# Performance work log

Measured on AMD Instinct MI355X. Metric: run time of the kernel, lower is better.

## Reference

```python
import jax, jax.numpy as jnp
import numpy as np

B, C, H, W = 32, 256, 56, 56
G, K, RED = 2, 7, 4
BN_EPS = 1e-5


def _conv2d(x, w, pad, groups=1, bias=None):
    # x: (N, Cin, H, W), w: (Cout, Cin/groups, kh, kw)
    y = jax.lax.conv_general_dilated(
        x, w, window_strides=(1, 1), padding=[(pad, pad), (pad, pad)],
        dimension_numbers=("NCHW", "OIHW", "NCHW"), feature_group_count=groups)
    if bias is not None:
        y = y + bias[None, :, None, None]
    return y


def setup_inputs() -> dict:
    key = jax.random.key(0)
    ks = jax.random.split(key, 5)
    return {
        "x": jax.random.normal(ks[0], (B, C, H, W), jnp.float32),
        "w_dyn": jax.random.normal(ks[1], (G, C, K, K), jnp.float32) * 0.02,
        "proj1_w": jax.random.normal(ks[2], (C // RED, C, 3, 3), jnp.float32) * 0.02,
        "bn_gamma": jnp.ones((C // RED,), jnp.float32),
        "bn_beta": jnp.zeros((C // RED,), jnp.float32),
        "proj2_w": jax.random.normal(ks[3], (C * G, C // RED, 3, 3), jnp.float32) * 0.02,
        "proj2_b": jnp.zeros((C * G,), jnp.float32),
    }


def reference(x, w_dyn, proj1_w, bn_gamma, bn_beta, proj2_w, proj2_b):
    b, c, h, w = x.shape
    # AdaptiveAvgPool2d((K, K)); H, W divisible by K -> exact mean over (H//K, W//K) windows
    pooled = x.reshape(b, c, K, h // K, K, w // K).mean(axis=(3, 5))  # (B, C, K, K)
    # proj: Conv3x3 (no bias, BN follows) -> BN (inference: mean=0, var=1) -> GELU -> Conv3x3
    hmid = _conv2d(pooled, proj1_w, pad=1)
    hmid = hmid * (bn_gamma / jnp.sqrt(1.0 + BN_EPS))[None, :, None, None] + bn_beta[None, :, None, None]
    hmid = jax.nn.gelu(hmid, approximate=False)
    scale = _conv2d(hmid, proj2_w, pad=1, bias=proj2_b)  # (B, G*C, K, K)
    scale = jax.nn.softmax(scale.reshape(b, G, c, K, K), axis=1)
    # per-sample dynamic depthwise kernel: softmax-weighted mix of G kernel banks
    dyn_w = jnp.einsum("bgckl,gckl->bckl", scale, w_dyn)  # (B, C, K, K)
    # depthwise conv with per-sample weights: groups = B*C
    y = _conv2d(x.reshape(1, b * c, h, w), dyn_w.reshape(b * c, 1, K, K),
                pad=K // 2, groups=b * c)
    return y.reshape(b, c, h, w)
```

## Files before the change

kernel.cpp:

```cpp
#include <hip/hip_runtime.h>
#include <math.h>

#define BB 32
#define CC 256
#define HH 56
#define WW 56
#define KP 49
#define CMID 64
#define HW 3136

#define RSTR 64
#define PROWS 62
#define PSZ (PROWS * RSTR)

__global__ __launch_bounds__(256) void pre_kernel(const float* __restrict__ x,
                                                  const float* __restrict__ w1,
                                                  const float* __restrict__ w2,
                                                  float* __restrict__ pooled,
                                                  float* __restrict__ w1t,
                                                  float* __restrict__ w2t) {
    int bid = blockIdx.x;
    if (bid < 2048) {
        int wv = threadIdx.x >> 6, lane = threadIdx.x & 63;
        int g = bid * 4 + wv;
        if (lane < KP) {
            int ko = lane / 7, kw = lane - ko * 7;
            const float* base = x + (size_t)g * HW + (ko * 8) * WW + kw * 8;
            float s = 0.f;
            #pragma unroll
            for (int r = 0; r < 8; ++r) {
                float4 a = *(const float4*)(base + r * WW);
                float4 b4 = *(const float4*)(base + r * WW + 4);
                s += a.x + a.y + a.z + a.w + b4.x + b4.y + b4.z + b4.w;
            }
            pooled[(size_t)g * KP + lane] = s * (1.f / 64.f);
        }
        return;
    }
    __shared__ float t[64][65];
    int r = threadIdx.x >> 6, c = threadIdx.x & 63;
    if (bid < 2048 + 36) {
        int ct0 = (bid - 2048) * 64;
        #pragma unroll
        for (int i = 0; i < 16; ++i)
            t[r + 4 * i][c] = w1[(size_t)(r + 4 * i) * 2304 + ct0 + c];
        __syncthreads();
        #pragma unroll
        for (int i = 0; i < 16; ++i)
            w1t[(size_t)(ct0 + r + 4 * i) * 64 + c] = t[c][r + 4 * i];
    } else {
        int tt = bid - 2048 - 36;
        int co0 = (tt / 9) * 64, ct0 = (tt % 9) * 64;
        #pragma unroll
        for (int i = 0; i < 16; ++i)
            t[r + 4 * i][c] = w2[(size_t)(co0 + r + 4 * i) * 576 + ct0 + c];
        __syncthreads();
        #pragma unroll
        for (int i = 0; i < 16; ++i)
            w2t[(size_t)(ct0 + r + 4 * i) * 512 + co0 + c] = t[c][r + 4 * i];
    }
}

__global__ __launch_bounds__(512) void conv1_kernel(const float* __restrict__ pooled,
                                                    const float* __restrict__ w1t,
                                                    const float* __restrict__ gamma,
                                                    const float* __restrict__ beta,
                                                    float* __restrict__ hmid) {
    int y = blockIdx.x, b = blockIdx.y;
    int wv = threadIdx.x >> 6, co = threadIdx.x & 63;
    __shared__ float red[8][7][64];
    float acc[7] = {0.f, 0.f, 0.f, 0.f, 0.f, 0.f, 0.f};
    const float* pb = pooled + (size_t)b * CC * KP;
    for (int ci = 0; ci < 32; ++ci) {
        int cin = wv * 32 + ci;
        const float* prow_base = pb + cin * KP;
        const float* wbase = w1t + (size_t)(cin * 9) * 64 + co;
        #pragma unroll
        for (int ky = 0; ky < 3; ++ky) {
            int iy = y + ky - 1;
            if (0 <= iy && iy < 7) {
                float s[9];
                s[0] = 0.f; s[8] = 0.f;
                const float* pr = prow_base + iy * 7;
                #pragma unroll
                for (int j = 0; j < 7; ++j) s[j + 1] = pr[j];
                const float* wr = wbase + ky * 3 * 64;
                float w0 = wr[0], w1v = wr[64], w2v = wr[128];
                #pragma unroll
                for (int xx = 0; xx < 7; ++xx)
                    acc[xx] += s[xx] * w0 + s[xx + 1] * w1v + s[xx + 2] * w2v;
            }
        }
    }
    #pragma unroll
    for (int xx = 0; xx < 7; ++xx) red[wv][xx][co] = acc[xx];
    __syncthreads();
    if (threadIdx.x < 448) {
        int xx = threadIdx.x >> 6, c2 = threadIdx.x & 63;
        float tot = 0.f;
        #pragma unroll
        for (int w = 0; w < 8; ++w) tot += red[w][xx][c2];
        float bnscale = gamma[c2] * rsqrtf(1.f + 1e-5f);
        float h = tot * bnscale + beta[c2];
        float g = 0.5f * h * (1.f + erff(h * 0.70710678118654752440f));
        hmid[((size_t)b * CMID + c2) * KP + y * 7 + xx] = g;
    }
}

__global__ __launch_bounds__(512) void conv2_kernel(const float* __restrict__ hmid,
                                                    const float* __restrict__ w2t,
                                                    const float* __restrict__ b2,
                                                    const float* __restrict__ wdyn,
                                                    float* __restrict__ dynw) {
    int y = blockIdx.x, b = blockIdx.y;
    int g = threadIdx.x >> 8, co = threadIdx.x & 255;
    __shared__ float redA[2][7][256];
    __shared__ float redB[2][7][256];
    float a0[7] = {}, a1[7] = {};
    const float* hb = hmid + (size_t)b * CMID * KP;
    for (int ci = 0; ci < 32; ++ci) {
        int cin = g * 32 + ci;
        const float* hrow_base = hb + cin * KP;
        const float* wbase = w2t + (size_t)(cin * 9) * 512 + co;
        #pragma unroll
        for (int ky = 0; ky < 3; ++ky) {
            int iy = y + ky - 1;
            if (0 <= iy && iy < 7) {
                float s[9];
                s[0] = 0.f; s[8] = 0.f;
                const float* hr = hrow_base + iy * 7;
                #pragma unroll
                for (int j = 0; j < 7; ++j) s[j + 1] = hr[j];
                const float* wr = wbase + ky * 3 * 512;
                float wa0 = wr[0],    wb0 = wr[256];
                float wa1 = wr[512],  wb1 = wr[768];
                float wa2 = wr[1024], wb2 = wr[1280];
                #pragma unroll
                for (int xx = 0; xx < 7; ++xx) {
                    float v0 = s[xx], v1 = s[xx + 1], v2 = s[xx + 2];
                    a0[xx] += v0 * wa0 + v1 * wa1 + v2 * wa2;
                    a1[xx] += v0 * wb0 + v1 * wb1 + v2 * wb2;
                }
            }
        }
    }
    #pragma unroll
    for (int xx = 0; xx < 7; ++xx) { redA[g][xx][co] = a0[xx]; redB[g][xx][co] = a1[xx]; }
    __syncthreads();
    if (threadIdx.x < 256) {
        int c = threadIdx.x;
        float bias0 = b2[c], bias1 = b2[c + CC];
        const float* wd0 = wdyn + (size_t)c * KP + y * 7;
        const float* wd1 = wdyn + (size_t)(CC + c) * KP + y * 7;
        float* dw = dynw + ((size_t)(b * CC + c)) * KP + y * 7;
        #pragma unroll
        for (int xx = 0; xx < 7; ++xx) {
            float s0 = redA[0][xx][c] + redA[1][xx][c] + bias0;
            float s1 = redB[0][xx][c] + redB[1][xx][c] + bias1;
            float m = fmaxf(s0, s1);
            float e0 = expf(s0 - m), e1 = expf(s1 - m);
            dw[xx] = (e0 * wd0[xx] + e1 * wd1[xx]) / (e0 + e1);
        }
    }
}

__global__ __launch_bounds__(64, 4) void dwconv_kernel(const float* __restrict__ x,
                                                       const float* __restrict__ dynw,
                                                       float* __restrict__ out) {
    __shared__ __align__(16) float xs[PSZ];
    int tid = threadIdx.x;
    int g = blockIdx.x;

    const float* wp = dynw + (size_t)g * KP;
    float w[49];
    #pragma unroll
    for (int i = 0; i < 49; ++i) w[i] = wp[i];

    for (int idx = tid; idx < 208; idx += 64) {
        int pr, col;
        if (idx < 96) {
            int rowi = idx >> 4, c4 = idx & 15;
            pr = rowi < 3 ? rowi : rowi + 56;
            col = 4 * c4;
        } else {
            int i = idx - 96;
            int rr = i >> 1;
            pr = rr + 3;
            int shift = 4 * (pr & 7);
            col = (i & 1) ? ((shift + 60) & 63) : shift;
        }
        *(float4*)(xs + pr * RSTR + col) = make_float4(0.f, 0.f, 0.f, 0.f);
    }

    for (int idx = tid; idx < 784; idx += 64) {
        int rr = idx / 14, c4 = idx - rr * 14;
        float4 v = *((const float4*)(x + (size_t)g * HW + rr * WW) + c4);
        int pr = rr + 3;
        int shift = 4 * (pr & 7);
        int col = (4 * c4 + 4 + shift) & 63;
        *(float4*)(xs + pr * RSTR + col) = v;
    }
    __syncthreads();

    if (tid < 56) {
        int ty = tid / 7, tx = tid - ty * 7;
        int r0 = 7 * ty, c0 = 8 * tx;
        float acc[7][8] = {};
        #pragma unroll
        for (int ir = 0; ir < 13; ++ir) {
            int pr = r0 + ir;
            int shift = 4 * (pr & 7);
            const float* rowp = xs + pr * RSTR;
            float rb[16];
            #pragma unroll
            for (int k = 0; k < 4; ++k) {
                int col = (c0 + shift + 4 * k) & 63;
                float4 v = *(const float4*)(rowp + col);
                rb[4 * k + 0] = v.x; rb[4 * k + 1] = v.y;
                rb[4 * k + 2] = v.z; rb[4 * k + 3] = v.w;
            }
            #pragma unroll
            for (int ky = 0; ky < 7; ++ky) {
                int oy = ir - ky;
                if (0 <= oy && oy < 7) {
                    #pragma unroll
                    for (int kx = 0; kx < 7; ++kx) {
                        float ww = w[ky * 7 + kx];
                        #pragma unroll
                        for (int ox = 0; ox < 8; ++ox)
                            acc[oy][ox] += rb[ox + 1 + kx] * ww;
                    }
                }
            }
        }
        float* op = out + (size_t)g * HW;
        #pragma unroll
        for (int oy = 0; oy < 7; ++oy) {
            float* orow = op + (r0 + oy) * WW + c0;
            *(float4*)(orow)     = make_float4(acc[oy][0], acc[oy][1], acc[oy][2], acc[oy][3]);
            *(float4*)(orow + 4) = make_float4(acc[oy][4], acc[oy][5], acc[oy][6], acc[oy][7]);
        }
    }
}

extern "C" void kernel_launch(void* const* d_in, const int* in_sizes, int n_in,
                              void* d_out, int out_size, void* d_ws, size_t ws_size,
                              hipStream_t stream) {
    const float* x     = (const float*)d_in[0];
    const float* wdyn  = (const float*)d_in[1];
    const float* w1    = (const float*)d_in[2];
    const float* gamma = (const float*)d_in[3];
    const float* beta  = (const float*)d_in[4];
    const float* w2    = (const float*)d_in[5];
    const float* b2    = (const float*)d_in[6];
    float* out = (float*)d_out;

    float* ws     = (float*)d_ws;
    float* pooled = ws;
    float* hmid   = ws + 401408;
    float* dynw   = ws + 501760;
    float* w1t    = ws + 903168;
    float* w2t    = ws + 1050624;

    pre_kernel   <<<dim3(2048 + 36 + 72), 256, 0, stream>>>(x, w1, w2, pooled, w1t, w2t);
    conv1_kernel <<<dim3(7, BB),          512, 0, stream>>>(pooled, w1t, gamma, beta, hmid);
    conv2_kernel <<<dim3(7, BB),          512, 0, stream>>>(hmid, w2t, b2, wdyn, dynw);
    dwconv_kernel<<<dim3(BB * CC),         64, 0, stream>>>(x, dynw, out);
}
```

Baseline: 321.0 us.

## Read depthwise input directly from global memory; double conv block threads

```diff
diff --git a/kernel.cpp b/kernel.cpp
--- a/kernel.cpp
+++ b/kernel.cpp
@@ -8,10 +8,6 @@
 #define KP 49
 #define CMID 64
 #define HW 3136
-
-#define RSTR 64
-#define PROWS 62
-#define PSZ (PROWS * RSTR)
 
 __global__ __launch_bounds__(256) void pre_kernel(const float* __restrict__ x,
                                                   const float* __restrict__ w1,
@@ -61,18 +57,20 @@
     }
 }
 
-__global__ __launch_bounds__(512) void conv1_kernel(const float* __restrict__ pooled,
-                                                    const float* __restrict__ w1t,
-                                                    const float* __restrict__ gamma,
-                                                    const float* __restrict__ beta,
-                                                    float* __restrict__ hmid) {
+__global__ __launch_bounds__(1024) void conv1_kernel(const float* __restrict__ pooled,
+                                                     const float* __restrict__ w1t,
+                                                     const float* __restrict__ gamma,
+                                                     const float* __restrict__ beta,
+                                                     float* __restrict__ hmid) {
     int y = blockIdx.x, b = blockIdx.y;
     int wv = threadIdx.x >> 6, co = threadIdx.x & 63;
-    __shared__ float red[8][7][64];
+    __shared__ float red[16][7][64];
     float acc[7] = {0.f, 0.f, 0.f, 0.f, 0.f, 0.f, 0.f};
     const float* pb = pooled + (size_t)b * CC * KP;
-    for (int ci = 0; ci < 32; ++ci) {
-        int cin = wv * 32 + ci;
+    int cin0 = __builtin_amdgcn_readfirstlane(wv * 16);
+    #pragma unroll 4
+    for (int ci = 0; ci < 16; ++ci) {
+        int cin = cin0 + ci;
         const float* prow_base = pb + cin * KP;
         const float* wbase = w1t + (size_t)(cin * 9) * 64 + co;
         #pragma unroll
@@ -99,7 +97,7 @@
         int xx = threadIdx.x >> 6, c2 = threadIdx.x & 63;
         float tot = 0.f;
         #pragma unroll
-        for (int w = 0; w < 8; ++w) tot += red[w][xx][c2];
+        for (int w = 0; w < 16; ++w) tot += red[w][xx][c2];
         float bnscale = gamma[c2] * rsqrtf(1.f + 1e-5f);
         float h = tot * bnscale + beta[c2];
         float g = 0.5f * h * (1.f + erff(h * 0.70710678118654752440f));
@@ -107,19 +105,21 @@
     }
 }
 
-__global__ __launch_bounds__(512) void conv2_kernel(const float* __restrict__ hmid,
-                                                    const float* __restrict__ w2t,
-                                                    const float* __restrict__ b2,
-                                                    const float* __restrict__ wdyn,
-                                                    float* __restrict__ dynw) {
+__global__ __launch_bounds__(1024) void conv2_kernel(const float* __restrict__ hmid,
+                                                     const float* __restrict__ w2t,
+                                                     const float* __restrict__ b2,
+                                                     const float* __restrict__ wdyn,
+                                                     float* __restrict__ dynw) {
     int y = blockIdx.x, b = blockIdx.y;
-    int g = threadIdx.x >> 8, co = threadIdx.x & 255;
-    __shared__ float redA[2][7][256];
-    __shared__ float redB[2][7][256];
+    int qq = threadIdx.x >> 8, co = threadIdx.x & 255;
+    __shared__ float redA[4][7][256];
+    __shared__ float redB[4][7][256];
     float a0[7] = {}, a1[7] = {};
     const float* hb = hmid + (size_t)b * CMID * KP;
-    for (int ci = 0; ci < 32; ++ci) {
-        int cin = g * 32 + ci;
+    int cin0 = __builtin_amdgcn_readfirstlane(qq * 16);
+    #pragma unroll 2
+    for (int ci = 0; ci < 16; ++ci) {
+        int cin = cin0 + ci;
         const float* hrow_base = hb + cin * KP;
         const float* wbase = w2t + (size_t)(cin * 9) * 512 + co;
         #pragma unroll
@@ -145,7 +145,7 @@
         }
     }
     #pragma unroll
-    for (int xx = 0; xx < 7; ++xx) { redA[g][xx][co] = a0[xx]; redB[g][xx][co] = a1[xx]; }
+    for (int xx = 0; xx < 7; ++xx) { redA[qq][xx][co] = a0[xx]; redB[qq][xx][co] = a1[xx]; }
     __syncthreads();
     if (threadIdx.x < 256) {
         int c = threadIdx.x;
@@ -155,8 +155,8 @@
         float* dw = dynw + ((size_t)(b * CC + c)) * KP + y * 7;
         #pragma unroll
         for (int xx = 0; xx < 7; ++xx) {
-            float s0 = redA[0][xx][c] + redA[1][xx][c] + bias0;
-            float s1 = redB[0][xx][c] + redB[1][xx][c] + bias1;
+            float s0 = redA[0][xx][c] + redA[1][xx][c] + redA[2][xx][c] + redA[3][xx][c] + bias0;
+            float s1 = redB[0][xx][c] + redB[1][xx][c] + redB[2][xx][c] + redB[3][xx][c] + bias1;
             float m = fmaxf(s0, s1);
             float e0 = expf(s0 - m), e1 = expf(s1 - m);
             dw[xx] = (e0 * wd0[xx] + e1 * wd1[xx]) / (e0 + e1);
@@ -167,7 +167,6 @@
 __global__ __launch_bounds__(64, 4) void dwconv_kernel(const float* __restrict__ x,
                                                        const float* __restrict__ dynw,
                                                        float* __restrict__ out) {
-    __shared__ __align__(16) float xs[PSZ];
     int tid = threadIdx.x;
     int g = blockIdx.x;
 
@@ -176,46 +175,24 @@
     #pragma unroll
     for (int i = 0; i < 49; ++i) w[i] = wp[i];
 
-    for (int idx = tid; idx < 208; idx += 64) {
-        int pr, col;
-        if (idx < 96) {
-            int rowi = idx >> 4, c4 = idx & 15;
-            pr = rowi < 3 ? rowi : rowi + 56;
-            col = 4 * c4;
-        } else {
-            int i = idx - 96;
-            int rr = i >> 1;
-            pr = rr + 3;
-            int shift = 4 * (pr & 7);
-            col = (i & 1) ? ((shift + 60) & 63) : shift;
-        }
-        *(float4*)(xs + pr * RSTR + col) = make_float4(0.f, 0.f, 0.f, 0.f);
-    }
-
-    for (int idx = tid; idx < 784; idx += 64) {
-        int rr = idx / 14, c4 = idx - rr * 14;
-        float4 v = *((const float4*)(x + (size_t)g * HW + rr * WW) + c4);
-        int pr = rr + 3;
-        int shift = 4 * (pr & 7);
-        int col = (4 * c4 + 4 + shift) & 63;
-        *(float4*)(xs + pr * RSTR + col) = v;
-    }
-    __syncthreads();
-
     if (tid < 56) {
         int ty = tid / 7, tx = tid - ty * 7;
         int r0 = 7 * ty, c0 = 8 * tx;
+        const float* xp = x + (size_t)g * HW;
         float acc[7][8] = {};
         #pragma unroll
         for (int ir = 0; ir < 13; ++ir) {
-            int pr = r0 + ir;
-            int shift = 4 * (pr & 7);
-            const float* rowp = xs + pr * RSTR;
+            int r = r0 + ir - 3;
+            bool rowok = (unsigned)r < 56u;
+            int rbase = r * WW;
             float rb[16];
             #pragma unroll
             for (int k = 0; k < 4; ++k) {
-                int col = (c0 + shift + 4 * k) & 63;
-                float4 v = *(const float4*)(rowp + col);
+                int w0 = c0 - 4 + 4 * k;
+                bool ok = rowok & ((unsigned)w0 < 56u);
+                int off = ok ? (rbase + w0) : 0;
+                float4 v = *(const float4*)(xp + off);
+                if (!ok) v = make_float4(0.f, 0.f, 0.f, 0.f);
                 rb[4 * k + 0] = v.x; rb[4 * k + 1] = v.y;
                 rb[4 * k + 2] = v.z; rb[4 * k + 3] = v.w;
             }
@@ -262,8 +239,8 @@
     float* w1t    = ws + 903168;
     float* w2t    = ws + 1050624;
 
-    pre_kernel   <<<dim3(2048 + 36 + 72), 256, 0, stream>>>(x, w1, w2, pooled, w1t, w2t);
-    conv1_kernel <<<dim3(7, BB),          512, 0, stream>>>(pooled, w1t, gamma, beta, hmid);
-    conv2_kernel <<<dim3(7, BB),          512, 0, stream>>>(hmid, w2t, b2, wdyn, dynw);
-    dwconv_kernel<<<dim3(BB * CC),         64, 0, stream>>>(x, dynw, out);
-}
+    pre_kernel   <<<dim3(2048 + 36 + 72),  256, 0, stream>>>(x, w1, w2, pooled, w1t, w2t);
+    conv1_kernel <<<dim3(7, BB),          1024, 0, stream>>>(pooled, w1t, gamma, beta, hmid);
+    conv2_kernel <<<dim3(7, BB),          1024, 0, stream>>>(hmid, w2t, b2, wdyn, dynw);
+    dwconv_kernel<<<dim3(BB * CC),          64, 0, stream>>>(x, dynw, out);
+}
```

New measurement: 282.2 us. 12.1% less time.
